# Optimization experiments

Measured on AMD Instinct MI355X. Metric: run time of the kernel, lower is better.

Reference implementation:

```python
import jax, jax.numpy as jnp
import numpy as np

B, SX, SY, D = 32, 2048, 2048, 160

def setup_inputs() -> dict:
    key = jax.random.key(0)
    ks = jax.random.split(key, 5)
    s = 1.0 / np.sqrt(D)
    return {
        "x": jax.random.normal(ks[0], (B, SX, D), dtype=jnp.float32),
        "y": jax.random.normal(ks[1], (B, SY, D), dtype=jnp.float32),
        "Wq": jax.random.normal(ks[2], (D, D), dtype=jnp.float32) * s,
        "bq": jnp.zeros((D,), dtype=jnp.float32),
        "Wk": jax.random.normal(ks[3], (D, D), dtype=jnp.float32) * s,
        "bk": jnp.zeros((D,), dtype=jnp.float32),
        "Wv": jax.random.normal(ks[4], (D, D), dtype=jnp.float32) * s,
        "bv": jnp.zeros((D,), dtype=jnp.float32),
    }

def reference(x, y, Wq, bq, Wk, bk, Wv, bv):
    # torch nn.Linear: out = in @ W.T + b, W is [out_dim, in_dim]
    q = jnp.einsum('bxd,ed->bxe', x, Wq) + bq          # [B,SX,D]
    k = jnp.einsum('byd,ed->bye', y, Wk) + bk          # [B,SY,D]
    v = jnp.einsum('byd,ed->bye', y, Wv) + bv          # [B,SY,D]
    scores = jnp.einsum('bxd,byd->bxy', q, k)          # [B,SX,SY] (no scaling in source)
    attn = jax.nn.softmax(scores, axis=-1)
    out = jnp.einsum('bxy,byd->bxd', attn, v)          # dropout is identity at eval
    return out + x                                     # residual
```

## Files before the change

kernel.cpp:

```cpp
#include <hip/hip_runtime.h>

#define LOG2E 1.44269504088896340736f

typedef _Float16 f16;
typedef __attribute__((ext_vector_type(2))) _Float16 f16x2;
typedef __attribute__((ext_vector_type(4))) _Float16 f16x4;
typedef __attribute__((ext_vector_type(8))) _Float16 f16x8;
typedef __attribute__((ext_vector_type(4))) float f32x4;
typedef __attribute__((ext_vector_type(16))) float f32x16;
typedef __attribute__((ext_vector_type(8))) unsigned short us8;

#define BB 32
#define SSX 2048
#define SSY 2048
#define DD 160
#define M_TOTAL (BB*SSX)

#define PRS 168
#define VTRS 136
#define RS 168

__device__ __forceinline__ f32x4 mfma16(f16x8 a, f16x8 b, f32x4 c) {
  return __builtin_amdgcn_mfma_f32_16x16x32_f16(a, b, c, 0, 0, 0);
}

__device__ __forceinline__ f32x16 mfma32(f16x8 a, f16x8 b, f32x16 c) {
  return __builtin_amdgcn_mfma_f32_32x32x16_f16(a, b, c, 0, 0, 0);
}

__device__ __forceinline__ unsigned pk2(float a, float b) {
  union { f16x2 h; unsigned u; } x;
  x.h = (f16x2){(f16)a, (f16)b};
  return x.u;
}

__global__ __launch_bounds__(256, 2) void proj_kernel(
    const float* __restrict__ x, const float* __restrict__ y,
    const float* __restrict__ Wq, const float* __restrict__ bq,
    const float* __restrict__ Wk, const float* __restrict__ bk,
    const float* __restrict__ Wv, const float* __restrict__ bv,
    f16* __restrict__ Qw, f16* __restrict__ Kw, f16* __restrict__ Vtw)
{
  __shared__ __align__(16) f16 buf[160*PRS];
  const int t = threadIdx.x;
  const int wave = t >> 6;
  const int lane = t & 63;
  const int quad = lane >> 4;
  const int l16  = lane & 15;
  const int bid  = blockIdx.x;
  const int kind = bid % 3;
  const int tile = bid / 3;
  const int row0 = tile * 128;
  const float* src  = (kind == 0) ? x  : y;
  const float* W    = (kind == 0) ? Wq : (kind == 1 ? Wk : Wv);
  const float* bias = (kind == 0) ? bq : (kind == 1 ? bk : bv);

  for (int i = 0; i < 20; ++i) {
    int idx = t + i*256;
    int r = idx / 40, c4 = idx % 40;
    float4 v = *(const float4*)&src[(size_t)(row0 + r)*DD + c4*4];
    f16x4 h = { (f16)v.x, (f16)v.y, (f16)v.z, (f16)v.w };
    *(f16x4*)&buf[r*PRS + c4*4] = h;
  }
  __syncthreads();
  f16x8 afr0[5], afr1[5];
  #pragma unroll
  for (int ks = 0; ks < 5; ++ks) {
    afr0[ks] = *(const f16x8*)&buf[(wave*32 + l16)*PRS + ks*32 + quad*8];
    afr1[ks] = *(const f16x8*)&buf[(wave*32 + 16 + l16)*PRS + ks*32 + quad*8];
  }
  __syncthreads();

  for (int i = 0; i < 25; ++i) {
    int idx = t + i*256;
    int r = idx / 40, c4 = idx % 40;
    float4 v = *(const float4*)&W[r*160 + c4*4];
    f16x4 h = { (f16)v.x, (f16)v.y, (f16)v.z, (f16)v.w };
    *(f16x4*)&buf[r*PRS + c4*4] = h;
  }
  __syncthreads();

  f32x4 acc0[10], acc1[10];
  #pragma unroll
  for (int nt = 0; nt < 10; ++nt) {
    float bs = bias[nt*16 + l16];
    acc0[nt] = (f32x4){bs,bs,bs,bs};
    acc1[nt] = (f32x4){bs,bs,bs,bs};
    #pragma unroll
    for (int ks = 0; ks < 5; ++ks) {
      f16x8 bfr = *(const f16x8*)&buf[(nt*16 + l16)*PRS + ks*32 + quad*8];
      acc0[nt] = mfma16(afr0[ks], bfr, acc0[nt]);
      acc1[nt] = mfma16(afr1[ks], bfr, acc1[nt]);
    }
  }
  __syncthreads();

  if (kind < 2) {
    f16* dst = (kind == 0) ? Qw : Kw;
    #pragma unroll
    for (int nt = 0; nt < 10; ++nt)
      #pragma unroll
      for (int r = 0; r < 4; ++r) {
        buf[(wave*32 + quad*4 + r)*PRS + nt*16 + l16]      = (f16)acc0[nt][r];
        buf[(wave*32 + 16 + quad*4 + r)*PRS + nt*16 + l16] = (f16)acc1[nt][r];
      }
    __syncthreads();
    for (int i = 0; i < 10; ++i) {
      int idx = t + i*256;
      int r = idx / 20, g = idx % 20;
      *(us8*)&dst[(size_t)(row0 + r)*DD + g*8] = *(const us8*)&buf[r*PRS + g*8];
    }
  } else {
    #pragma unroll
    for (int nt = 0; nt < 10; ++nt)
      #pragma unroll
      for (int r = 0; r < 4; ++r) {
        buf[(nt*16 + l16)*VTRS + wave*32 + quad*4 + r]      = (f16)acc0[nt][r];
        buf[(nt*16 + l16)*VTRS + wave*32 + 16 + quad*4 + r] = (f16)acc1[nt][r];
      }
    __syncthreads();
    const int b  = row0 / SSY;
    const int y0 = row0 % SSY;
    for (int i = 0; i < 10; ++i) {
      int idx = t + i*256;
      int d = idx / 16, yg = idx % 16;
      *(us8*)&Vtw[((size_t)b*DD + d)*SSY + y0 + yg*8] = *(const us8*)&buf[d*VTRS + yg*8];
    }
  }
}


#define LOAD_CHUNK(yb) { \
  const f16* ksrc = Kw + ((size_t)b*SSY + (yb))*DD; \
  const f16* vsrc = Vtw + (size_t)b*DD*SSY + (yb); \
  _Pragma("unroll") \
  for (int i = 0; i < 5; ++i) { \
    int idx = t + i*256; int r = idx/20, c = idx%20; \
    kreg[i] = *(const us8*)&ksrc[(size_t)r*DD + c*8]; \
  } \
  _Pragma("unroll") \
  for (int i = 0; i < 5; ++i) { \
    int idx = t + i*256; int d = idx>>3, g = idx&7; \
    vreg[i] = *(const us8*)&vsrc[(size_t)d*SSY + g*8]; \
  } \
}

#define STORE_CHUNK() { \
  _Pragma("unroll") \
  for (int i = 0; i < 5; ++i) { \
    int idx = t + i*256; int r = idx/20, c = idx%20; \
    *(us8*)&K_lds[r*RS + c*8] = kreg[i]; \
  } \
  _Pragma("unroll") \
  for (int i = 0; i < 5; ++i) { \
    int idx = t + i*256; int d = idx>>3, g = idx&7; \
    *(us8*)&Vt_lds[d*64 + ((g ^ (d & 7)) << 3)] = vreg[i]; \
  } \
}

__global__ __launch_bounds__(256, 2) void flash_kernel(
    const f16* __restrict__ Qw, const f16* __restrict__ Kw, const f16* __restrict__ Vtw,
    const float* __restrict__ x, float* __restrict__ out)
{
  __shared__ __align__(16) f16 K_lds[64*RS];
  __shared__ __align__(16) f16 Vt_lds[160*64];
  const int t = threadIdx.x;
  const int wave = t >> 6;
  const int lane = t & 63;
  const int l31  = lane & 31;
  const int hi   = lane >> 5;
  const int bid  = blockIdx.x;
  const int b    = bid >> 4;
  const int x0   = (bid & 15) * 128;

  f16x8 qfr[10];
  #pragma unroll
  for (int h = 0; h < 2; ++h) {
    if (h) __syncthreads();
    const f16* qsrc = Qw + ((size_t)b*SSX + x0 + h*64)*DD;
    for (int i = 0; i < 5; ++i) {
      int idx = t + i*256;
      int r = idx / 20, c = idx % 20;
      *(us8*)&K_lds[r*RS + c*8] = *(const us8*)&qsrc[(size_t)r*DD + c*8];
    }
    __syncthreads();
    if ((wave >> 1) == h) {
      const int base = (wave & 1)*32;
      #pragma unroll
      for (int s = 0; s < 10; ++s)
        qfr[s] = *(const f16x8*)&K_lds[(base + l31)*RS + s*16 + hi*8];
    }
  }

  f32x16 acc[5];
  #pragma unroll
  for (int i = 0; i < 5; ++i)
    #pragma unroll
    for (int r = 0; r < 16; ++r) acc[i][r] = 0.f;
  float m = -1e30f, l = 0.f;

  us8 kreg[5], vreg[5];
  LOAD_CHUNK(0);

  for (int yc = 0; yc < SSY/64; ++yc) {
    __syncthreads();
    STORE_CHUNK();
    __syncthreads();
    if (yc < SSY/64 - 1) LOAD_CHUNK((yc+1)*64);

    f32x16 S0, S1;
    #pragma unroll
    for (int r = 0; r < 16; ++r) { S0[r] = 0.f; S1[r] = 0.f; }
    __builtin_amdgcn_s_setprio(1);
    #pragma unroll
    for (int s = 0; s < 10; ++s) {
      f16x8 k0 = *(const f16x8*)&K_lds[l31*RS + s*16 + hi*8];
      f16x8 k1 = *(const f16x8*)&K_lds[(32 + l31)*RS + s*16 + hi*8];
      S0 = mfma32(k0, qfr[s], S0);
      S1 = mfma32(k1, qfr[s], S1);
    }
    __builtin_amdgcn_s_setprio(0);

    float pmax = S0[0];
    #pragma unroll
    for (int r = 1; r < 16; ++r) pmax = fmaxf(pmax, S0[r]);
    #pragma unroll
    for (int r = 0; r < 16; ++r) pmax = fmaxf(pmax, S1[r]);
    pmax = fmaxf(pmax, __shfl_xor(pmax, 32));

    if (__any(pmax > m + 8.f)) {
      float n  = fmaxf(m, pmax);
      float sc = exp2f((m - n)*LOG2E);
      m = n; l *= sc;
      #pragma unroll
      for (int r = 0; r < 16; ++r) {
        float scq = __shfl(sc, (r&3) + 8*(r>>2) + 4*hi);
        #pragma unroll
        for (int dt = 0; dt < 5; ++dt) acc[dt][r] *= scq;
      }
    }

    float lsum = 0.f;
    #pragma unroll
    for (int r = 0; r < 16; ++r) { S0[r] = exp2f((S0[r] - m)*LOG2E); lsum += S0[r]; }
    #pragma unroll
    for (int r = 0; r < 16; ++r) { S1[r] = exp2f((S1[r] - m)*LOG2E); lsum += S1[r]; }
    lsum += __shfl_xor(lsum, 32);
    l += lsum;

    #pragma unroll
    for (int c = 0; c < 4; ++c) {
      const int bo = (c & 1)*8;
      unsigned L0, L1, H0, H1;
      if (c < 2) {
        L0 = pk2(S0[bo+0], S0[bo+1]); L1 = pk2(S0[bo+2], S0[bo+3]);
        H0 = pk2(S0[bo+4], S0[bo+5]); H1 = pk2(S0[bo+6], S0[bo+7]);
      } else {
        L0 = pk2(S1[bo+0], S1[bo+1]); L1 = pk2(S1[bo+2], S1[bo+3]);
        H0 = pk2(S1[bo+4], S1[bo+5]); H1 = pk2(S1[bo+6], S1[bo+7]);
      }
      unsigned sd0 = hi ? L0 : H0;
      unsigned sd1 = hi ? L1 : H1;
      unsigned rc0 = (unsigned)__shfl_xor((int)sd0, 32);
      unsigned rc1 = (unsigned)__shfl_xor((int)sd1, 32);
      union { unsigned u[4]; f16x8 h; } pw;
      pw.u[0] = hi ? rc0 : L0;
      pw.u[1] = hi ? rc1 : L1;
      pw.u[2] = hi ? H0 : rc0;
      pw.u[3] = hi ? H1 : rc1;
      __builtin_amdgcn_s_setprio(1);
      #pragma unroll
      for (int dt = 0; dt < 5; ++dt) {
        int row = dt*32 + l31;
        f16x8 vf = *(const f16x8*)&Vt_lds[row*64 + (((c*2 + hi) ^ (row & 7)) << 3)];
        acc[dt] = mfma32(pw.h, vf, acc[dt]);
      }
      __builtin_amdgcn_s_setprio(0);
    }
  }

  #pragma unroll
  for (int r = 0; r < 16; ++r) {
    int qr = (r&3) + 8*(r>>2) + 4*hi;
    float rl = 1.f / __shfl(l, qr);
    size_t rowoff = ((size_t)b*SSX + x0 + wave*32 + qr)*DD + l31;
    #pragma unroll
    for (int dt = 0; dt < 5; ++dt) {
      size_t o = rowoff + (size_t)dt*32;
      out[o] = acc[dt][r]*rl + x[o];
    }
  }
}

extern "C" void kernel_launch(void* const* d_in, const int* in_sizes, int n_in,
                              void* d_out, int out_size, void* d_ws, size_t ws_size,
                              hipStream_t stream) {
  const float* x  = (const float*)d_in[0];
  const float* y  = (const float*)d_in[1];
  const float* Wq = (const float*)d_in[2];
  const float* bq = (const float*)d_in[3];
  const float* Wk = (const float*)d_in[4];
  const float* bk = (const float*)d_in[5];
  const float* Wv = (const float*)d_in[6];
  const float* bv = (const float*)d_in[7];

  f16* Qw  = (f16*)d_ws;
  f16* Kw  = Qw + (size_t)M_TOTAL*DD;
  f16* Vtw = Kw + (size_t)M_TOTAL*DD;

  proj_kernel<<<1536, 256, 0, stream>>>(x, y, Wq, bq, Wk, bk, Wv, bv, Qw, Kw, Vtw);
  flash_kernel<<<512, 256, 0, stream>>>(Qw, Kw, Vtw, x, (float*)d_out);
}
```

Before: 299.4 us.

## Double-buffer K/V tiles in LDS with XOR swizzle and remapped block order

The flash kernel now keeps two LDS buffers for K and Vt, so the next chunk is written to the spare buffer while the current one is consumed, and there is one barrier per iteration instead of two. The K layout drops its row padding in favour of an XOR swizzle to avoid bank conflicts, and loads are issued two chunks ahead. Block indices in both kernels are permuted to spread work across XCDs, and the projection kernel's launch bounds allow 3 blocks per CU. The doubled LDS use may reduce flash kernel occupancy.

```diff
diff --git a/kernel.cpp b/kernel.cpp
--- a/kernel.cpp
+++ b/kernel.cpp
@@ -18,7 +18,7 @@
 
 #define PRS 168
 #define VTRS 136
-#define RS 168
+#define KST 160
 
 __device__ __forceinline__ f32x4 mfma16(f16x8 a, f16x8 b, f32x4 c) {
   return __builtin_amdgcn_mfma_f32_16x16x32_f16(a, b, c, 0, 0, 0);
@@ -34,7 +34,7 @@
   return x.u;
 }
 
-__global__ __launch_bounds__(256, 2) void proj_kernel(
+__global__ __launch_bounds__(256, 3) void proj_kernel(
     const float* __restrict__ x, const float* __restrict__ y,
     const float* __restrict__ Wq, const float* __restrict__ bq,
     const float* __restrict__ Wk, const float* __restrict__ bk,
@@ -47,7 +47,7 @@
   const int lane = t & 63;
   const int quad = lane >> 4;
   const int l16  = lane & 15;
-  const int bid  = blockIdx.x;
+  const int bid  = (blockIdx.x & 7) * 192 + (blockIdx.x >> 3);
   const int kind = bid % 3;
   const int tile = bid / 3;
   const int row0 = tile * 128;
@@ -145,16 +145,16 @@
   } \
 }
 
-#define STORE_CHUNK() { \
+#define STORE_CHUNK(cb) { \
   _Pragma("unroll") \
   for (int i = 0; i < 5; ++i) { \
     int idx = t + i*256; int r = idx/20, c = idx%20; \
-    *(us8*)&K_lds[r*RS + c*8] = kreg[i]; \
+    *(us8*)&K_lds[cb][r*KST + ((c ^ ((r>>1)&3))<<3)] = kreg[i]; \
   } \
   _Pragma("unroll") \
   for (int i = 0; i < 5; ++i) { \
     int idx = t + i*256; int d = idx>>3, g = idx&7; \
-    *(us8*)&Vt_lds[d*64 + ((g ^ (d & 7)) << 3)] = vreg[i]; \
+    *(us8*)&Vt_lds[cb][d*64 + ((g ^ (d & 7))<<3)] = vreg[i]; \
   } \
 }
 
@@ -162,16 +162,20 @@
     const f16* __restrict__ Qw, const f16* __restrict__ Kw, const f16* __restrict__ Vtw,
     const float* __restrict__ x, float* __restrict__ out)
 {
-  __shared__ __align__(16) f16 K_lds[64*RS];
-  __shared__ __align__(16) f16 Vt_lds[160*64];
+  __shared__ __align__(16) f16 K_lds[2][64*KST];
+  __shared__ __align__(16) f16 Vt_lds[2][160*64];
   const int t = threadIdx.x;
   const int wave = t >> 6;
   const int lane = t & 63;
   const int l31  = lane & 31;
   const int hi   = lane >> 5;
-  const int bid  = blockIdx.x;
+  const int bid  = (blockIdx.x & 7) * 64 + (blockIdx.x >> 3);
   const int b    = bid >> 4;
   const int x0   = (bid & 15) * 128;
+  const int rot  = (l31 >> 1) & 3;
+
+  us8 kreg[5], vreg[5];
+  LOAD_CHUNK(0);
 
   f16x8 qfr[10];
   #pragma unroll
@@ -181,16 +185,17 @@
     for (int i = 0; i < 5; ++i) {
       int idx = t + i*256;
       int r = idx / 20, c = idx % 20;
-      *(us8*)&K_lds[r*RS + c*8] = *(const us8*)&qsrc[(size_t)r*DD + c*8];
+      *(us8*)&K_lds[0][r*KST + ((c ^ ((r>>1)&3))<<3)] = *(const us8*)&qsrc[(size_t)r*DD + c*8];
     }
     __syncthreads();
     if ((wave >> 1) == h) {
       const int base = (wave & 1)*32;
       #pragma unroll
       for (int s = 0; s < 10; ++s)
-        qfr[s] = *(const f16x8*)&K_lds[(base + l31)*RS + s*16 + hi*8];
-    }
-  }
+        qfr[s] = *(const f16x8*)&K_lds[0][(base + l31)*KST + (((s*2 + hi) ^ rot)<<3)];
+    }
+  }
+  __syncthreads();
 
   f32x16 acc[5];
   #pragma unroll
@@ -199,14 +204,14 @@
     for (int r = 0; r < 16; ++r) acc[i][r] = 0.f;
   float m = -1e30f, l = 0.f;
 
-  us8 kreg[5], vreg[5];
-  LOAD_CHUNK(0);
+  STORE_CHUNK(0);
+  LOAD_CHUNK(64);
+  __syncthreads();
 
   for (int yc = 0; yc < SSY/64; ++yc) {
-    __syncthreads();
-    STORE_CHUNK();
-    __syncthreads();
-    if (yc < SSY/64 - 1) LOAD_CHUNK((yc+1)*64);
+    const int cur = yc & 1;
+    const f16* Kc = K_lds[cur];
+    const f16* Vc = Vt_lds[cur];
 
     f32x16 S0, S1;
     #pragma unroll
@@ -214,18 +219,21 @@
     __builtin_amdgcn_s_setprio(1);
     #pragma unroll
     for (int s = 0; s < 10; ++s) {
-      f16x8 k0 = *(const f16x8*)&K_lds[l31*RS + s*16 + hi*8];
-      f16x8 k1 = *(const f16x8*)&K_lds[(32 + l31)*RS + s*16 + hi*8];
+      f16x8 k0 = *(const f16x8*)&Kc[l31*KST + (((s*2 + hi) ^ rot)<<3)];
+      f16x8 k1 = *(const f16x8*)&Kc[(32 + l31)*KST + (((s*2 + hi) ^ rot)<<3)];
       S0 = mfma32(k0, qfr[s], S0);
       S1 = mfma32(k1, qfr[s], S1);
     }
     __builtin_amdgcn_s_setprio(0);
 
-    float pmax = S0[0];
-    #pragma unroll
-    for (int r = 1; r < 16; ++r) pmax = fmaxf(pmax, S0[r]);
-    #pragma unroll
-    for (int r = 0; r < 16; ++r) pmax = fmaxf(pmax, S1[r]);
+    if (yc < SSY/64 - 1) STORE_CHUNK(cur ^ 1);
+    if (yc < SSY/64 - 2) LOAD_CHUNK((yc+2)*64);
+
+    float pmax = fmaxf(S0[0], S0[1]);
+    #pragma unroll
+    for (int r = 2; r < 16; r += 2) pmax = fmaxf(pmax, fmaxf(S0[r], S0[r+1]));
+    #pragma unroll
+    for (int r = 0; r < 16; r += 2) pmax = fmaxf(pmax, fmaxf(S1[r], S1[r+1]));
     pmax = fmaxf(pmax, __shfl_xor(pmax, 32));
 
     if (__any(pmax > m + 8.f)) {
@@ -272,11 +280,13 @@
       #pragma unroll
       for (int dt = 0; dt < 5; ++dt) {
         int row = dt*32 + l31;
-        f16x8 vf = *(const f16x8*)&Vt_lds[row*64 + (((c*2 + hi) ^ (row & 7)) << 3)];
+        f16x8 vf = *(const f16x8*)&Vc[row*64 + (((c*2 + hi) ^ (row & 7)) << 3)];
         acc[dt] = mfma32(pw.h, vf, acc[dt]);
       }
       __builtin_amdgcn_s_setprio(0);
     }
+
+    __syncthreads();
   }
 
   #pragma unroll
```

Result: slower. 313.4 us (+4.6%).
